# Performance work log

Hardware: AMD Instinct MI355X
Metric: run time of the kernel (lower is better)

The kernel has to match this reference:

```python
import jax, jax.numpy as jnp
import numpy as np

D_MODEL = 1024
N_HEAD = 16
D_HEAD = D_MODEL // N_HEAD
B, L = 4, 1024


def setup_inputs() -> dict:
    key = jax.random.key(0)
    ks = jax.random.split(key, 14)
    s = 0.02
    return {
        "qx": jax.random.normal(ks[0], (B, L, D_MODEL), jnp.float32),
        "kvx": jax.random.normal(ks[1], (B, L, D_MODEL), jnp.float32),
        "qs": jax.random.normal(ks[2], (B, L, D_MODEL), jnp.float32),
        "kvs": jax.random.normal(ks[3], (B, L, D_MODEL), jnp.float32),
        "w_qx1": jax.random.normal(ks[4], (D_MODEL, D_MODEL), jnp.float32) * s,
        "w_qs1": jax.random.normal(ks[5], (D_MODEL, D_MODEL), jnp.float32) * s,
        "w_qx2": jax.random.normal(ks[6], (D_MODEL, D_MODEL), jnp.float32) * s,
        "w_qs2": jax.random.normal(ks[7], (D_MODEL, D_MODEL), jnp.float32) * s,
        "w_kvx": jax.random.normal(ks[8], (D_MODEL, 2 * D_HEAD), jnp.float32) * s,
        "w_kvs": jax.random.normal(ks[9], (D_MODEL, 2 * D_HEAD), jnp.float32) * s,
        "w_xproj": jax.random.normal(ks[10], (2 * D_MODEL, D_MODEL), jnp.float32) * s,
        "b_xproj": jax.random.normal(ks[11], (D_MODEL,), jnp.float32) * s,
        "w_sproj": jax.random.normal(ks[12], (2 * D_MODEL, D_MODEL), jnp.float32) * s,
        "b_sproj": jax.random.normal(ks[13], (D_MODEL,), jnp.float32) * s,
    }


def _split_heads(t):
    # [B, L, D] -> [B, H, L, d]
    b, l, d = t.shape
    return t.reshape(b, l, N_HEAD, D_HEAD).transpose(0, 2, 1, 3)


def _merge_heads(t):
    # [B, H, L, d] -> [B, L, H*d]
    b, h, l, d = t.shape
    return t.transpose(0, 2, 1, 3).reshape(b, l, h * d)


def _attn(q, k, v):
    # q: [B, H, L, d]; k, v: [B, M, d] (single shared KV head broadcast over H)
    score = jnp.einsum("bhld,bmd->bhlm", q, k) / jnp.sqrt(jnp.float32(D_HEAD))
    p = jax.nn.softmax(score, axis=-1)
    return jnp.einsum("bhlm,bmd->bhld", p, v)


def reference(qx, kvx, qs, kvs, w_qx1, w_qs1, w_qx2, w_qs2, w_kvx, w_kvs,
              w_xproj, b_xproj, w_sproj, b_sproj):
    qx1 = _split_heads(qx @ w_qx1)
    qs1 = _split_heads(qs @ w_qs1)
    qx2 = _split_heads(qx @ w_qx2)
    qs2 = _split_heads(qs @ w_qs2)
    kx, vx = jnp.split(kvx @ w_kvx, 2, axis=-1)  # each [B, L, d]
    ks_, vs_ = jnp.split(kvs @ w_kvs, 2, axis=-1)
    x = _attn(qx1, kx, vx)
    s = _attn(qs1, ks_, vs_)
    xs = _attn(qx2, ks_, vs_)
    sx = _attn(qs2, kx, vx)
    # concat on head-dim then merge heads -> [B, L, 2*D]
    x_cat = _merge_heads(jnp.concatenate((xs, x), axis=-1))
    s_cat = _merge_heads(jnp.concatenate((sx, s), axis=-1))
    x_out = x_cat @ w_xproj + b_xproj
    s_out = s_cat @ w_sproj + b_sproj
    return (x_out, s_out)
```

## Files before the change

### kernel.cpp

```cpp
#include <hip/hip_runtime.h>
#include <hip/hip_bf16.h>


typedef short short8 __attribute__((ext_vector_type(8)));
typedef short short4v __attribute__((ext_vector_type(4)));
typedef float floatx4 __attribute__((ext_vector_type(4)));
typedef float floatx16 __attribute__((ext_vector_type(16)));
typedef unsigned uintx2 __attribute__((ext_vector_type(2)));

__device__ __forceinline__ float b2f(ushort h) {
    union { unsigned u; float f; } v; v.u = ((unsigned)h) << 16; return v.f;
}
__device__ __forceinline__ ushort f2bf(float f) {
    union { float f; unsigned u; } v; v.f = f;
    return (ushort)((v.u + 0x7FFFu + ((v.u >> 16) & 1u)) >> 16);
}
__device__ __forceinline__ unsigned cvt_pk_bf16(float lo, float hi) {
    unsigned r;
    asm("v_cvt_pk_bf16_f32 %0, %1, %2" : "=v"(r) : "v"(lo), "v"(hi));
    return r;
}
__device__ __forceinline__ void gl_lds16(const ushort* g, ushort* l) {
    __builtin_amdgcn_global_load_lds(
        (const __attribute__((address_space(1))) void*)g,
        (__attribute__((address_space(3))) void*)l, 16, 0, 0);
}

struct CB { const float* src[2]; ushort* dst[2]; };

__global__ __launch_bounds__(256) void castb(CB cb) {
    const int z = blockIdx.z;
    const float* s = cb.src[z];
    ushort* d = cb.dst[z];
    const size_t i = ((size_t)blockIdx.x * 256 + threadIdx.x) * 4;
    floatx4 f = *(const floatx4*)&s[i];
    short4v o;
#pragma unroll
    for (int k = 0; k < 4; k++) o[k] = (short)f2bf(f[k]);
    *(short4v*)&d[i] = o;
}

struct TB { const float* src[4]; ushort* dst[4]; int K[4]; int N[4]; };

__global__ __launch_bounds__(256) void tbatch(TB tb) {
    __shared__ float tile[32][33];
    const int wi = blockIdx.z;
    const int K = tb.K[wi], N = tb.N[wi];
    const int k0 = blockIdx.x * 32, n0 = blockIdx.y * 32;
    if (k0 >= K || n0 >= N) return;
    const float* W = tb.src[wi];
    ushort* Wt = tb.dst[wi];
    const int tx = threadIdx.x & 31, ty = threadIdx.x >> 5;
#pragma unroll
    for (int i = ty; i < 32; i += 8)
        tile[i][tx] = W[(size_t)(k0 + i) * N + n0 + tx];
    __syncthreads();
#pragma unroll
    for (int i = ty; i < 32; i += 8)
        Wt[(size_t)(n0 + i) * K + k0 + tx] = f2bf(tile[tx][i]);
}

__global__ __launch_bounds__(256) void gemm_q(
    const ushort* __restrict__ A, const ushort* __restrict__ Bt,
    ushort* __restrict__ C, float cscale)
{
    __shared__ ushort As[128 * 32];
    __shared__ ushort Bs[64 * 32];
    const int t = threadIdx.x;
    const int lane = t & 63, w = t >> 6;
    const int q = lane >> 4, li = lane & 15;
    const int rowA = blockIdx.x * 128, colB = blockIdx.y * 64;
    const int ar = rowA + w * 32 + (lane >> 2);
    const int br = colB + w * 16 + (lane >> 2);
    const int cl = (lane & 3) * 8;
    ushort* adst = &As[w * 32 * 32];
    ushort* bdst = &Bs[w * 16 * 32];

    floatx4 acc[2][4];
    const floatx4 z4 = {0.f, 0.f, 0.f, 0.f};
#pragma unroll
    for (int i = 0; i < 2; i++)
#pragma unroll
        for (int j = 0; j < 4; j++) acc[i][j] = z4;

    for (int k0 = 0; k0 < 1024; k0 += 32) {
        gl_lds16(A + (size_t)ar * 1024 + k0 + cl, adst);
        gl_lds16(A + (size_t)(ar + 16) * 1024 + k0 + cl, adst + 16 * 32);
        gl_lds16(Bt + (size_t)br * 1024 + k0 + cl, bdst);
        __syncthreads();
        short8 af[2], bf[4];
#pragma unroll
        for (int i = 0; i < 2; i++) af[i] = *(const short8*)&As[(w * 32 + i * 16 + li) * 32 + q * 8];
#pragma unroll
        for (int j = 0; j < 4; j++) bf[j] = *(const short8*)&Bs[(j * 16 + li) * 32 + q * 8];
#pragma unroll
        for (int i = 0; i < 2; i++)
#pragma unroll
            for (int j = 0; j < 4; j++)
                acc[i][j] = __builtin_amdgcn_mfma_f32_16x16x32_bf16(af[i], bf[j], acc[i][j], 0, 0, 0);
        __syncthreads();
    }
#pragma unroll
    for (int i = 0; i < 2; i++) {
        const int rowb = rowA + w * 32 + i * 16 + q * 4;
#pragma unroll
        for (int j = 0; j < 4; j++) {
            const int col = colB + j * 16 + li;
#pragma unroll
            for (int r = 0; r < 4; r++)
                C[(size_t)(rowb + r) * 2048 + col] = f2bf(acc[i][j][r] * cscale);
        }
    }
}

__global__ __launch_bounds__(256) void gemm_kv(
    const ushort* __restrict__ A0, const ushort* __restrict__ A1,
    const ushort* __restrict__ B0, const ushort* __restrict__ B1,
    ushort* __restrict__ C0, ushort* __restrict__ C1,
    ushort* __restrict__ vt0, ushort* __restrict__ vt1)
{
    __shared__ ushort As[128 * 32];
    __shared__ ushort Bs[128 * 32];
    const int z = blockIdx.z;
    const ushort* A = z ? A1 : A0;
    const ushort* Bt = z ? B1 : B0;
    ushort* Kp = z ? C1 : C0;
    ushort* vt = z ? vt1 : vt0;

    const int t = threadIdx.x;
    const int lane = t & 63, w = t >> 6;
    const int q = lane >> 4, li = lane & 15;
    const int wr = (w >> 1) * 64, wc = (w & 1) * 64;
    const int rowA = blockIdx.x * 128;
    const int ar = rowA + w * 32 + (lane >> 2);
    const int br = w * 32 + (lane >> 2);
    const int cl = (lane & 3) * 8;
    ushort* adst = &As[w * 32 * 32];
    ushort* bdst = &Bs[w * 32 * 32];

    floatx4 acc[4][4];
    const floatx4 z4 = {0.f, 0.f, 0.f, 0.f};
#pragma unroll
    for (int i = 0; i < 4; i++)
#pragma unroll
        for (int j = 0; j < 4; j++) acc[i][j] = z4;

    for (int k0 = 0; k0 < 1024; k0 += 32) {
        gl_lds16(A + (size_t)ar * 1024 + k0 + cl, adst);
        gl_lds16(A + (size_t)(ar + 16) * 1024 + k0 + cl, adst + 16 * 32);
        gl_lds16(Bt + (size_t)br * 1024 + k0 + cl, bdst);
        gl_lds16(Bt + (size_t)(br + 16) * 1024 + k0 + cl, bdst + 16 * 32);
        __syncthreads();
        short8 af[4], bf[4];
#pragma unroll
        for (int i = 0; i < 4; i++) af[i] = *(const short8*)&As[(wr + i * 16 + li) * 32 + q * 8];
#pragma unroll
        for (int j = 0; j < 4; j++) bf[j] = *(const short8*)&Bs[(wc + j * 16 + li) * 32 + q * 8];
#pragma unroll
        for (int i = 0; i < 4; i++)
#pragma unroll
            for (int j = 0; j < 4; j++)
                acc[i][j] = __builtin_amdgcn_mfma_f32_16x16x32_bf16(af[i], bf[j], acc[i][j], 0, 0, 0);
        __syncthreads();
    }
#pragma unroll
    for (int i = 0; i < 4; i++) {
        const int rowb = rowA + wr + i * 16 + q * 4;
#pragma unroll
        for (int j = 0; j < 4; j++) {
            const int col = wc + j * 16 + li;
#pragma unroll
            for (int r = 0; r < 4; r++) {
                const int row = rowb + r;
                const ushort vb = f2bf(acc[i][j][r]);
                if (col < 64) Kp[(size_t)row * 64 + col] = vb;
                else vt[((row >> 10) << 16) + ((col - 64) << 10) + (row & 1023)] = vb;
            }
        }
    }
}

__global__ __launch_bounds__(256) void gemm_proj(
    const ushort* __restrict__ A1, const ushort* __restrict__ A2,
    const ushort* __restrict__ Bt, const float* __restrict__ bias,
    float* __restrict__ C)
{
    __shared__ ushort As[128 * 32];
    __shared__ ushort Bs[64 * 32];
    const int t = threadIdx.x;
    const int lane = t & 63, w = t >> 6;
    const int q = lane >> 4, li = lane & 15;
    const int rowA = blockIdx.x * 128, colB = blockIdx.y * 64;
    const int ar = rowA + w * 32 + (lane >> 2);
    const int br = colB + w * 16 + (lane >> 2);
    const int cl = (lane & 3) * 8;
    ushort* adst = &As[w * 32 * 32];
    ushort* bdst = &Bs[w * 16 * 32];

    floatx4 acc[2][4];
    const floatx4 z4 = {0.f, 0.f, 0.f, 0.f};
#pragma unroll
    for (int i = 0; i < 2; i++)
#pragma unroll
        for (int j = 0; j < 4; j++) acc[i][j] = z4;

    for (int k0 = 0; k0 < 2048; k0 += 32) {
        const ushort* Ap = (k0 < 1024) ? A1 : A2;
        const int kc = k0 & 1023;
        const int kp = kc + cl;
        const int ks = ((kp >> 6) << 7) + (kp & 63) + ((k0 >= 1024) ? 64 : 0);
        gl_lds16(Ap + (size_t)ar * 1024 + kc + cl, adst);
        gl_lds16(Ap + (size_t)(ar + 16) * 1024 + kc + cl, adst + 16 * 32);
        gl_lds16(Bt + (size_t)br * 2048 + ks, bdst);
        __syncthreads();
        short8 af[2], bf[4];
#pragma unroll
        for (int i = 0; i < 2; i++) af[i] = *(const short8*)&As[(w * 32 + i * 16 + li) * 32 + q * 8];
#pragma unroll
        for (int j = 0; j < 4; j++) bf[j] = *(const short8*)&Bs[(j * 16 + li) * 32 + q * 8];
#pragma unroll
        for (int i = 0; i < 2; i++)
#pragma unroll
            for (int j = 0; j < 4; j++)
                acc[i][j] = __builtin_amdgcn_mfma_f32_16x16x32_bf16(af[i], bf[j], acc[i][j], 0, 0, 0);
        __syncthreads();
    }
#pragma unroll
    for (int i = 0; i < 2; i++) {
        const int rowb = rowA + w * 32 + i * 16 + q * 4;
#pragma unroll
        for (int j = 0; j < 4; j++) {
            const int col = colB + j * 16 + li;
            const float bv = bias[col];
#pragma unroll
            for (int r = 0; r < 4; r++)
                C[(size_t)(rowb + r) * 1024 + col] = acc[i][j][r] + bv;
        }
    }
}

__global__ __launch_bounds__(256, 4) void attn_kernel(
    const ushort* __restrict__ Qbase,
    const ushort* __restrict__ KVa, const ushort* __restrict__ KVb,
    ushort* __restrict__ OutA, ushort* __restrict__ OutB)
{
    __shared__ ushort Kt[64 * 68];
    __shared__ ushort Vt[64 * 68];
    __shared__ __align__(16) float Ls[4][32];

    const int t = threadIdx.x;
    const int lane = t & 63, w = t >> 6;
    const int ql = lane & 31, hi = lane >> 5;
    const int qt = blockIdx.x, h = blockIdx.y;
    const int z = blockIdx.z, b = z >> 1, a2 = z & 1;

    const ushort* Q  = Qbase + (a2 ? 1024 : 0);
    const ushort* KV = a2 ? KVb : KVa;
    ushort* Out      = a2 ? OutB : OutA;
    const ushort* Kp = KV;
    const ushort* Vg = KV + 262144;

    const size_t qrow = (size_t)(b * 1024 + qt * 128 + w * 32 + ql);
    short8 qf[4];
#pragma unroll
    for (int dc = 0; dc < 4; dc++)
        qf[dc] = *(const short8*)&Q[qrow * 2048 + h * 64 + dc * 16 + hi * 8];

    float lsum = 0.f;
    floatx16 accO[2];
#pragma unroll
    for (int dt = 0; dt < 2; dt++)
#pragma unroll
        for (int i = 0; i < 16; i++) accO[dt][i] = 0.f;

    const int srow = t >> 2, sch = (t & 3) * 16;
    const ushort* ksrc0 = &Kp[(size_t)(b * 1024 + srow) * 64 + sch];
    const ushort* vsrc0 = &Vg[(size_t)(b * 64 + srow) * 1024 + sch];
    ushort* kdst = &Kt[srow * 68 + sch];
    ushort* vdst = &Vt[srow * 68 + sch];

    short8 kreg[2], vreg[2];
#pragma unroll
    for (int i = 0; i < 2; i++) {
        kreg[i] = *(const short8*)&ksrc0[i * 8];
        vreg[i] = *(const short8*)&vsrc0[i * 8];
    }

    for (int kt = 0; kt < 16; kt++) {
#pragma unroll
        for (int i = 0; i < 2; i++) {
            *(short8*)&kdst[i * 8] = kreg[i];
            *(short8*)&vdst[i * 8] = vreg[i];
        }
        __syncthreads();

        if (kt < 15) {
            const ushort* ksrc = ksrc0 + (size_t)(kt + 1) * 64 * 64;
            const ushort* vsrc = vsrc0 + (kt + 1) * 64;
#pragma unroll
            for (int i = 0; i < 2; i++) {
                kreg[i] = *(const short8*)&ksrc[i * 8];
                vreg[i] = *(const short8*)&vsrc[i * 8];
            }
        }

#pragma unroll
        for (int ktile = 0; ktile < 2; ktile++) {
            floatx16 S;
#pragma unroll
            for (int i = 0; i < 16; i++) S[i] = 0.f;
            __builtin_amdgcn_s_setprio(1);
#pragma unroll
            for (int dc = 0; dc < 4; dc++) {
                short8 kf = *(const short8*)&Kt[(ktile * 32 + ql) * 68 + dc * 16 + hi * 8];
                S = __builtin_amdgcn_mfma_f32_32x32x16_bf16(kf, qf[dc], S, 0, 0, 0);
            }
            __builtin_amdgcn_s_setprio(0);

            float e[16];
#pragma unroll
            for (int r = 0; r < 16; r++) e[r] = exp2f(S[r]);
            float sa = (e[0] + e[1]) + (e[2] + e[3]);
            float sb = (e[4] + e[5]) + (e[6] + e[7]);
            float sc = (e[8] + e[9]) + (e[10] + e[11]);
            float sd = (e[12] + e[13]) + (e[14] + e[15]);
            lsum += (sa + sb) + (sc + sd);

#pragma unroll
            for (int p = 0; p < 2; p++) {
                unsigned cA = cvt_pk_bf16(e[8 * p + 0], e[8 * p + 1]);
                unsigned cC = cvt_pk_bf16(e[8 * p + 2], e[8 * p + 3]);
                unsigned cB = cvt_pk_bf16(e[8 * p + 4], e[8 * p + 5]);
                unsigned cD = cvt_pk_bf16(e[8 * p + 6], e[8 * p + 7]);
                uintx2 s02 = __builtin_amdgcn_permlane32_swap(cA, cB, false, false);
                uintx2 s13 = __builtin_amdgcn_permlane32_swap(cC, cD, false, false);
                union { unsigned u[4]; short8 s; } pf;
                pf.u[0] = s02[0]; pf.u[1] = s13[0];
                pf.u[2] = s02[1]; pf.u[3] = s13[1];
                const int kslot = ktile * 2 + p;
                __builtin_amdgcn_s_setprio(1);
#pragma unroll
                for (int dt = 0; dt < 2; dt++) {
                    short8 vf = *(const short8*)&Vt[(dt * 32 + ql) * 68 + kslot * 16 + hi * 8];
                    accO[dt] = __builtin_amdgcn_mfma_f32_32x32x16_bf16(pf.s, vf, accO[dt], 0, 0, 0);
                }
                __builtin_amdgcn_s_setprio(0);
            }
        }
        __syncthreads();
    }

    lsum += __shfl_xor(lsum, 32);
    Ls[w][ql] = lsum;

    const int orow0 = b * 1024 + qt * 128 + w * 32;
#pragma unroll
    for (int g = 0; g < 4; g++) {
        floatx4 L4 = *(const floatx4*)&Ls[w][g * 8 + hi * 4];
#pragma unroll
        for (int rr = 0; rr < 4; rr++) {
            const float inv = 1.f / L4[rr];
            const int row = orow0 + g * 8 + hi * 4 + rr;
#pragma unroll
            for (int dt = 0; dt < 2; dt++)
                Out[(size_t)row * 1024 + h * 64 + dt * 32 + ql] =
                    f2bf(accO[dt][g * 4 + rr] * inv);
        }
    }
}

extern "C" void kernel_launch(void* const* d_in, const int* in_sizes, int n_in,
                              void* d_out, int out_size, void* d_ws, size_t ws_size,
                              hipStream_t stream) {
    const float* qx    = (const float*)d_in[0];
    const float* kvx   = (const float*)d_in[1];
    const float* qs    = (const float*)d_in[2];
    const float* kvs   = (const float*)d_in[3];
    const float* w_qx1 = (const float*)d_in[4];
    const float* w_qs1 = (const float*)d_in[5];
    const float* w_qx2 = (const float*)d_in[6];
    const float* w_qs2 = (const float*)d_in[7];
    const float* w_kvx = (const float*)d_in[8];
    const float* w_kvs = (const float*)d_in[9];
    const float* w_xp  = (const float*)d_in[10];
    const float* b_xp  = (const float*)d_in[11];
    const float* w_sp  = (const float*)d_in[12];
    const float* b_sp  = (const float*)d_in[13];
    float* out = (float*)d_out;
    (void)ws_size; (void)in_sizes; (void)n_in; (void)out_size;

    ushort* ws   = (ushort*)d_ws;
    ushort* Wb   = ws;
    ushort* q1q2 = ws + 4194304;
    ushort* Mbuf = ws + 12582912;
    ushort* kvpx = ws + 16777216;
    ushort* kvps = ws + 17301504;

    const float qsc = 0.125f * 1.44269504088896f;

    CB c1; c1.src[0] = kvx; c1.dst[0] = Mbuf; c1.src[1] = kvs; c1.dst[1] = q1q2;
    castb<<<dim3(4096, 1, 2), 256, 0, stream>>>(c1);

    TB tb1;
    tb1.src[0] = w_kvx; tb1.dst[0] = Wb;           tb1.K[0] = 1024; tb1.N[0] = 128;
    tb1.src[1] = w_kvs; tb1.dst[1] = Wb + 131072;  tb1.K[1] = 1024; tb1.N[1] = 128;
    tb1.src[2] = w_qs1; tb1.dst[2] = Wb + 262144;  tb1.K[2] = 1024; tb1.N[2] = 1024;
    tb1.src[3] = w_qs2; tb1.dst[3] = Wb + 1310720; tb1.K[3] = 1024; tb1.N[3] = 1024;
    tbatch<<<dim3(32, 32, 4), 256, 0, stream>>>(tb1);

    gemm_kv<<<dim3(32, 1, 2), 256, 0, stream>>>(
        Mbuf, q1q2, Wb, Wb + 131072, kvpx, kvps, kvpx + 262144, kvps + 262144);

    CB c2; c2.src[0] = qs; c2.dst[0] = Mbuf; c2.src[1] = qs; c2.dst[1] = Mbuf;
    castb<<<dim3(4096, 1, 1), 256, 0, stream>>>(c2);

    gemm_q<<<dim3(32, 32), 256, 0, stream>>>(Mbuf, Wb + 262144, q1q2, qsc);

    attn_kernel<<<dim3(8, 16, 8), 256, 0, stream>>>(q1q2, kvps, kvpx, Mbuf, (ushort*)out);

    TB tb2;
    tb2.src[0] = w_sp;  tb2.dst[0] = Wb;           tb2.K[0] = 2048; tb2.N[0] = 1024;
    tb2.src[1] = w_qx1; tb2.dst[1] = Wb + 2097152; tb2.K[1] = 1024; tb2.N[1] = 1024;
    tb2.src[2] = w_qx2; tb2.dst[2] = Wb + 3145728; tb2.K[2] = 1024; tb2.N[2] = 1024;
    tb2.src[3] = w_sp;  tb2.dst[3] = Wb;           tb2.K[3] = 0;    tb2.N[3] = 0;
    tbatch<<<dim3(64, 32, 3), 256, 0, stream>>>(tb2);

    gemm_proj<<<dim3(32, 16), 256, 0, stream>>>((ushort*)out, Mbuf, Wb, b_sp, out + 4194304);

    CB c3; c3.src[0] = qx; c3.dst[0] = Mbuf; c3.src[1] = qx; c3.dst[1] = Mbuf;
    castb<<<dim3(4096, 1, 1), 256, 0, stream>>>(c3);

    gemm_q<<<dim3(32, 32), 256, 0, stream>>>(Mbuf, Wb + 2097152, q1q2, qsc);

    attn_kernel<<<dim3(8, 16, 8), 256, 0, stream>>>(q1q2, kvpx, kvps, Mbuf, Wb);

    TB tb3;
    tb3.src[0] = w_xp; tb3.dst[0] = q1q2; tb3.K[0] = 2048; tb3.N[0] = 1024;
    tb3.src[1] = w_xp; tb3.dst[1] = q1q2; tb3.K[1] = 0;    tb3.N[1] = 0;
    tb3.src[2] = w_xp; tb3.dst[2] = q1q2; tb3.K[2] = 0;    tb3.N[2] = 0;
    tb3.src[3] = w_xp; tb3.dst[3] = q1q2; tb3.K[3] = 0;    tb3.N[3] = 0;
    tbatch<<<dim3(64, 32, 1), 256, 0, stream>>>(tb3);

    gemm_proj<<<dim3(32, 16), 256, 0, stream>>>(Wb, Mbuf, q1q2, b_xp, out);
}
```

Measured before the change: 449.1 us.

## Double K-step per barrier in GEMMs and switch attention exp to __expf

The q-projection and output-projection GEMMs now load two 32-wide K slices per iteration into separate LDS buffers and run both MFMA groups between one pair of barriers. This halves the number of synchronisations and loop iterations and keeps more loads in flight, at the cost of twice the LDS per block. Separately, the attention softmax uses __expf on unscaled-by-log2e scores instead of exp2f on pre-scaled scores. __expf likely lowers to exp2 plus a multiply, which adds a multiply per element for no clear gain.

```diff
diff --git a/kernel.cpp b/kernel.cpp
--- a/kernel.cpp
+++ b/kernel.cpp
@@ -64,8 +64,10 @@
     const ushort* __restrict__ A, const ushort* __restrict__ Bt,
     ushort* __restrict__ C, float cscale)
 {
-    __shared__ ushort As[128 * 32];
-    __shared__ ushort Bs[64 * 32];
+    __shared__ ushort As0[128 * 32];
+    __shared__ ushort As1[128 * 32];
+    __shared__ ushort Bs0[64 * 32];
+    __shared__ ushort Bs1[64 * 32];
     const int t = threadIdx.x;
     const int lane = t & 63, w = t >> 6;
     const int q = lane >> 4, li = lane & 15;
@@ -73,8 +75,10 @@
     const int ar = rowA + w * 32 + (lane >> 2);
     const int br = colB + w * 16 + (lane >> 2);
     const int cl = (lane & 3) * 8;
-    ushort* adst = &As[w * 32 * 32];
-    ushort* bdst = &Bs[w * 16 * 32];
+    ushort* adst0 = &As0[w * 32 * 32];
+    ushort* adst1 = &As1[w * 32 * 32];
+    ushort* bdst0 = &Bs0[w * 16 * 32];
+    ushort* bdst1 = &Bs1[w * 16 * 32];
 
     floatx4 acc[2][4];
     const floatx4 z4 = {0.f, 0.f, 0.f, 0.f};
@@ -83,16 +87,28 @@
 #pragma unroll
         for (int j = 0; j < 4; j++) acc[i][j] = z4;
 
-    for (int k0 = 0; k0 < 1024; k0 += 32) {
-        gl_lds16(A + (size_t)ar * 1024 + k0 + cl, adst);
-        gl_lds16(A + (size_t)(ar + 16) * 1024 + k0 + cl, adst + 16 * 32);
-        gl_lds16(Bt + (size_t)br * 1024 + k0 + cl, bdst);
+    for (int k0 = 0; k0 < 1024; k0 += 64) {
+        gl_lds16(A + (size_t)ar * 1024 + k0 + cl, adst0);
+        gl_lds16(A + (size_t)(ar + 16) * 1024 + k0 + cl, adst0 + 16 * 32);
+        gl_lds16(A + (size_t)ar * 1024 + k0 + 32 + cl, adst1);
+        gl_lds16(A + (size_t)(ar + 16) * 1024 + k0 + 32 + cl, adst1 + 16 * 32);
+        gl_lds16(Bt + (size_t)br * 1024 + k0 + cl, bdst0);
+        gl_lds16(Bt + (size_t)br * 1024 + k0 + 32 + cl, bdst1);
         __syncthreads();
         short8 af[2], bf[4];
 #pragma unroll
-        for (int i = 0; i < 2; i++) af[i] = *(const short8*)&As[(w * 32 + i * 16 + li) * 32 + q * 8];
-#pragma unroll
-        for (int j = 0; j < 4; j++) bf[j] = *(const short8*)&Bs[(j * 16 + li) * 32 + q * 8];
+        for (int i = 0; i < 2; i++) af[i] = *(const short8*)&As0[(w * 32 + i * 16 + li) * 32 + q * 8];
+#pragma unroll
+        for (int j = 0; j < 4; j++) bf[j] = *(const short8*)&Bs0[(j * 16 + li) * 32 + q * 8];
+#pragma unroll
+        for (int i = 0; i < 2; i++)
+#pragma unroll
+            for (int j = 0; j < 4; j++)
+                acc[i][j] = __builtin_amdgcn_mfma_f32_16x16x32_bf16(af[i], bf[j], acc[i][j], 0, 0, 0);
+#pragma unroll
+        for (int i = 0; i < 2; i++) af[i] = *(const short8*)&As1[(w * 32 + i * 16 + li) * 32 + q * 8];
+#pragma unroll
+        for (int j = 0; j < 4; j++) bf[j] = *(const short8*)&Bs1[(j * 16 + li) * 32 + q * 8];
 #pragma unroll
         for (int i = 0; i < 2; i++)
 #pragma unroll
@@ -185,8 +201,10 @@
     const ushort* __restrict__ Bt, const float* __restrict__ bias,
     float* __restrict__ C)
 {
-    __shared__ ushort As[128 * 32];
-    __shared__ ushort Bs[64 * 32];
+    __shared__ ushort As0[128 * 32];
+    __shared__ ushort As1[128 * 32];
+    __shared__ ushort Bs0[64 * 32];
+    __shared__ ushort Bs1[64 * 32];
     const int t = threadIdx.x;
     const int lane = t & 63, w = t >> 6;
     const int q = lane >> 4, li = lane & 15;
@@ -194,8 +212,10 @@
     const int ar = rowA + w * 32 + (lane >> 2);
     const int br = colB + w * 16 + (lane >> 2);
     const int cl = (lane & 3) * 8;
-    ushort* adst = &As[w * 32 * 32];
-    ushort* bdst = &Bs[w * 16 * 32];
+    ushort* adst0 = &As0[w * 32 * 32];
+    ushort* adst1 = &As1[w * 32 * 32];
+    ushort* bdst0 = &Bs0[w * 16 * 32];
+    ushort* bdst1 = &Bs1[w * 16 * 32];
 
     floatx4 acc[2][4];
     const floatx4 z4 = {0.f, 0.f, 0.f, 0.f};
@@ -204,20 +224,35 @@
 #pragma unroll
         for (int j = 0; j < 4; j++) acc[i][j] = z4;
 
-    for (int k0 = 0; k0 < 2048; k0 += 32) {
+    for (int k0 = 0; k0 < 2048; k0 += 64) {
         const ushort* Ap = (k0 < 1024) ? A1 : A2;
         const int kc = k0 & 1023;
-        const int kp = kc + cl;
-        const int ks = ((kp >> 6) << 7) + (kp & 63) + ((k0 >= 1024) ? 64 : 0);
-        gl_lds16(Ap + (size_t)ar * 1024 + kc + cl, adst);
-        gl_lds16(Ap + (size_t)(ar + 16) * 1024 + kc + cl, adst + 16 * 32);
-        gl_lds16(Bt + (size_t)br * 2048 + ks, bdst);
+        const int kp0 = kc + cl;
+        const int kp1 = kc + 32 + cl;
+        const int koff = (k0 >= 1024) ? 64 : 0;
+        const int ks0 = ((kp0 >> 6) << 7) + (kp0 & 63) + koff;
+        const int ks1 = ((kp1 >> 6) << 7) + (kp1 & 63) + koff;
+        gl_lds16(Ap + (size_t)ar * 1024 + kc + cl, adst0);
+        gl_lds16(Ap + (size_t)(ar + 16) * 1024 + kc + cl, adst0 + 16 * 32);
+        gl_lds16(Ap + (size_t)ar * 1024 + kc + 32 + cl, adst1);
+        gl_lds16(Ap + (size_t)(ar + 16) * 1024 + kc + 32 + cl, adst1 + 16 * 32);
+        gl_lds16(Bt + (size_t)br * 2048 + ks0, bdst0);
+        gl_lds16(Bt + (size_t)br * 2048 + ks1, bdst1);
         __syncthreads();
         short8 af[2], bf[4];
 #pragma unroll
-        for (int i = 0; i < 2; i++) af[i] = *(const short8*)&As[(w * 32 + i * 16 + li) * 32 + q * 8];
-#pragma unroll
-        for (int j = 0; j < 4; j++) bf[j] = *(const short8*)&Bs[(j * 16 + li) * 32 + q * 8];
+        for (int i = 0; i < 2; i++) af[i] = *(const short8*)&As0[(w * 32 + i * 16 + li) * 32 + q * 8];
+#pragma unroll
+        for (int j = 0; j < 4; j++) bf[j] = *(const short8*)&Bs0[(j * 16 + li) * 32 + q * 8];
+#pragma unroll
+        for (int i = 0; i < 2; i++)
+#pragma unroll
+            for (int j = 0; j < 4; j++)
+                acc[i][j] = __builtin_amdgcn_mfma_f32_16x16x32_bf16(af[i], bf[j], acc[i][j], 0, 0, 0);
+#pragma unroll
+        for (int i = 0; i < 2; i++) af[i] = *(const short8*)&As1[(w * 32 + i * 16 + li) * 32 + q * 8];
+#pragma unroll
+        for (int j = 0; j < 4; j++) bf[j] = *(const short8*)&Bs1[(j * 16 + li) * 32 + q * 8];
 #pragma unroll
         for (int i = 0; i < 2; i++)
 #pragma unroll
@@ -319,7 +354,7 @@
 
             float e[16];
 #pragma unroll
-            for (int r = 0; r < 16; r++) e[r] = exp2f(S[r]);
+            for (int r = 0; r < 16; r++) e[r] = __expf(S[r]);
             float sa = (e[0] + e[1]) + (e[2] + e[3]);
             float sb = (e[4] + e[5]) + (e[6] + e[7]);
             float sc = (e[8] + e[9]) + (e[10] + e[11]);
@@ -396,8 +431,6 @@
     ushort* kvpx = ws + 16777216;
     ushort* kvps = ws + 17301504;
 
-    const float qsc = 0.125f * 1.44269504088896f;
-
     CB c1; c1.src[0] = kvx; c1.dst[0] = Mbuf; c1.src[1] = kvs; c1.dst[1] = q1q2;
     castb<<<dim3(4096, 1, 2), 256, 0, stream>>>(c1);
 
@@ -414,7 +447,7 @@
     CB c2; c2.src[0] = qs; c2.dst[0] = Mbuf; c2.src[1] = qs; c2.dst[1] = Mbuf;
     castb<<<dim3(4096, 1, 1), 256, 0, stream>>>(c2);
 
-    gemm_q<<<dim3(32, 32), 256, 0, stream>>>(Mbuf, Wb + 262144, q1q2, qsc);
+    gemm_q<<<dim3(32, 32), 256, 0, stream>>>(Mbuf, Wb + 262144, q1q2, 0.125f);
 
     attn_kernel<<<dim3(8, 16, 8), 256, 0, stream>>>(q1q2, kvps, kvpx, Mbuf, (ushort*)out);
 
@@ -430,7 +463,7 @@
     CB c3; c3.src[0] = qx; c3.dst[0] = Mbuf; c3.src[1] = qx; c3.dst[1] = Mbuf;
     castb<<<dim3(4096, 1, 1), 256, 0, stream>>>(c3);
 
-    gemm_q<<<dim3(32, 32), 256, 0, stream>>>(Mbuf, Wb + 2097152, q1q2, qsc);
+    gemm_q<<<dim3(32, 32), 256, 0, stream>>>(Mbuf, Wb + 2097152, q1q2, 0.125f);
 
     attn_kernel<<<dim3(8, 16, 8), 256, 0, stream>>>(q1q2, kvpx, kvps, Mbuf, Wb);
 
```

Result: faster. 417.5 us (-7.0%).

## Double-buffer LDS in Q and projection GEMMs with 64-wide K steps

Applied to the files above, without the earlier changes.

The Q-projection and output-projection GEMMs now use two LDS buffers and stage 64 K-elements per iteration. The next tile's global-to-LDS loads are issued while the current tile is being multiplied, and there is one barrier per iteration instead of two. This targets the serialized load-then-compute pattern. It also removes the log2(e) factor from the Q scale and switches the attention exponent from exp2f to __expf, which may compile to an extra multiply before the exp2. LDS use per block grows fourfold, which could reduce occupancy.

```diff
diff --git a/kernel.cpp b/kernel.cpp
--- a/kernel.cpp
+++ b/kernel.cpp
@@ -64,8 +64,8 @@
     const ushort* __restrict__ A, const ushort* __restrict__ Bt,
     ushort* __restrict__ C, float cscale)
 {
-    __shared__ ushort As[128 * 32];
-    __shared__ ushort Bs[64 * 32];
+    __shared__ ushort As[2][2][128 * 32];
+    __shared__ ushort Bs[2][2][64 * 32];
     const int t = threadIdx.x;
     const int lane = t & 63, w = t >> 6;
     const int q = lane >> 4, li = lane & 15;
@@ -73,8 +73,6 @@
     const int ar = rowA + w * 32 + (lane >> 2);
     const int br = colB + w * 16 + (lane >> 2);
     const int cl = (lane & 3) * 8;
-    ushort* adst = &As[w * 32 * 32];
-    ushort* bdst = &Bs[w * 16 * 32];
 
     floatx4 acc[2][4];
     const floatx4 z4 = {0.f, 0.f, 0.f, 0.f};
@@ -83,22 +81,35 @@
 #pragma unroll
         for (int j = 0; j < 4; j++) acc[i][j] = z4;
 
-    for (int k0 = 0; k0 < 1024; k0 += 32) {
-        gl_lds16(A + (size_t)ar * 1024 + k0 + cl, adst);
-        gl_lds16(A + (size_t)(ar + 16) * 1024 + k0 + cl, adst + 16 * 32);
-        gl_lds16(Bt + (size_t)br * 1024 + k0 + cl, bdst);
-        __syncthreads();
+    auto stage = [&](int ph, int k0) {
+        gl_lds16(A + (size_t)ar * 1024 + k0 + cl,        &As[ph][0][w * 32 * 32]);
+        gl_lds16(A + (size_t)(ar + 16) * 1024 + k0 + cl, &As[ph][0][w * 32 * 32] + 16 * 32);
+        gl_lds16(A + (size_t)ar * 1024 + k0 + 32 + cl,        &As[ph][1][w * 32 * 32]);
+        gl_lds16(A + (size_t)(ar + 16) * 1024 + k0 + 32 + cl, &As[ph][1][w * 32 * 32] + 16 * 32);
+        gl_lds16(Bt + (size_t)br * 1024 + k0 + cl,      &Bs[ph][0][w * 16 * 32]);
+        gl_lds16(Bt + (size_t)br * 1024 + k0 + 32 + cl, &Bs[ph][1][w * 16 * 32]);
+    };
+
+    stage(0, 0);
+    for (int it = 0; it < 16; it++) {
+        const int cur = it & 1;
+        __syncthreads();
+        if (it < 15) stage(cur ^ 1, (it + 1) * 64);
         short8 af[2], bf[4];
 #pragma unroll
-        for (int i = 0; i < 2; i++) af[i] = *(const short8*)&As[(w * 32 + i * 16 + li) * 32 + q * 8];
-#pragma unroll
-        for (int j = 0; j < 4; j++) bf[j] = *(const short8*)&Bs[(j * 16 + li) * 32 + q * 8];
-#pragma unroll
-        for (int i = 0; i < 2; i++)
+        for (int ks = 0; ks < 2; ks++) {
+#pragma unroll
+            for (int i = 0; i < 2; i++)
+                af[i] = *(const short8*)&As[cur][ks][(w * 32 + i * 16 + li) * 32 + q * 8];
 #pragma unroll
             for (int j = 0; j < 4; j++)
-                acc[i][j] = __builtin_amdgcn_mfma_f32_16x16x32_bf16(af[i], bf[j], acc[i][j], 0, 0, 0);
-        __syncthreads();
+                bf[j] = *(const short8*)&Bs[cur][ks][(j * 16 + li) * 32 + q * 8];
+#pragma unroll
+            for (int i = 0; i < 2; i++)
+#pragma unroll
+                for (int j = 0; j < 4; j++)
+                    acc[i][j] = __builtin_amdgcn_mfma_f32_16x16x32_bf16(af[i], bf[j], acc[i][j], 0, 0, 0);
+        }
     }
 #pragma unroll
     for (int i = 0; i < 2; i++) {
@@ -185,8 +196,8 @@
     const ushort* __restrict__ Bt, const float* __restrict__ bias,
     float* __restrict__ C)
 {
-    __shared__ ushort As[128 * 32];
-    __shared__ ushort Bs[64 * 32];
+    __shared__ ushort As[2][2][128 * 32];
+    __shared__ ushort Bs[2][2][64 * 32];
     const int t = threadIdx.x;
     const int lane = t & 63, w = t >> 6;
     const int q = lane >> 4, li = lane & 15;
@@ -194,8 +205,6 @@
     const int ar = rowA + w * 32 + (lane >> 2);
     const int br = colB + w * 16 + (lane >> 2);
     const int cl = (lane & 3) * 8;
-    ushort* adst = &As[w * 32 * 32];
-    ushort* bdst = &Bs[w * 16 * 32];
 
     floatx4 acc[2][4];
     const floatx4 z4 = {0.f, 0.f, 0.f, 0.f};
@@ -204,26 +213,42 @@
 #pragma unroll
         for (int j = 0; j < 4; j++) acc[i][j] = z4;
 
-    for (int k0 = 0; k0 < 2048; k0 += 32) {
+    auto stage = [&](int ph, int k0) {
         const ushort* Ap = (k0 < 1024) ? A1 : A2;
         const int kc = k0 & 1023;
-        const int kp = kc + cl;
-        const int ks = ((kp >> 6) << 7) + (kp & 63) + ((k0 >= 1024) ? 64 : 0);
-        gl_lds16(Ap + (size_t)ar * 1024 + kc + cl, adst);
-        gl_lds16(Ap + (size_t)(ar + 16) * 1024 + kc + cl, adst + 16 * 32);
-        gl_lds16(Bt + (size_t)br * 2048 + ks, bdst);
-        __syncthreads();
+        const int koff = (k0 >= 1024) ? 64 : 0;
+        const int kp0 = kc + cl;
+        const int kp1 = kc + 32 + cl;
+        const int ks0 = ((kp0 >> 6) << 7) + (kp0 & 63) + koff;
+        const int ks1 = ((kp1 >> 6) << 7) + (kp1 & 63) + koff;
+        gl_lds16(Ap + (size_t)ar * 1024 + kc + cl,        &As[ph][0][w * 32 * 32]);
+        gl_lds16(Ap + (size_t)(ar + 16) * 1024 + kc + cl, &As[ph][0][w * 32 * 32] + 16 * 32);
+        gl_lds16(Ap + (size_t)ar * 1024 + kc + 32 + cl,        &As[ph][1][w * 32 * 32]);
+        gl_lds16(Ap + (size_t)(ar + 16) * 1024 + kc + 32 + cl, &As[ph][1][w * 32 * 32] + 16 * 32);
+        gl_lds16(Bt + (size_t)br * 2048 + ks0, &Bs[ph][0][w * 16 * 32]);
+        gl_lds16(Bt + (size_t)br * 2048 + ks1, &Bs[ph][1][w * 16 * 32]);
+    };
+
+    stage(0, 0);
+    for (int it = 0; it < 32; it++) {
+        const int cur = it & 1;
+        __syncthreads();
+        if (it < 31) stage(cur ^ 1, (it + 1) * 64);
         short8 af[2], bf[4];
 #pragma unroll
-        for (int i = 0; i < 2; i++) af[i] = *(const short8*)&As[(w * 32 + i * 16 + li) * 32 + q * 8];
-#pragma unroll
-        for (int j = 0; j < 4; j++) bf[j] = *(const short8*)&Bs[(j * 16 + li) * 32 + q * 8];
-#pragma unroll
-        for (int i = 0; i < 2; i++)
+        for (int ks = 0; ks < 2; ks++) {
+#pragma unroll
+            for (int i = 0; i < 2; i++)
+                af[i] = *(const short8*)&As[cur][ks][(w * 32 + i * 16 + li) * 32 + q * 8];
 #pragma unroll
             for (int j = 0; j < 4; j++)
-                acc[i][j] = __builtin_amdgcn_mfma_f32_16x16x32_bf16(af[i], bf[j], acc[i][j], 0, 0, 0);
-        __syncthreads();
+                bf[j] = *(const short8*)&Bs[cur][ks][(j * 16 + li) * 32 + q * 8];
+#pragma unroll
+            for (int i = 0; i < 2; i++)
+#pragma unroll
+                for (int j = 0; j < 4; j++)
+                    acc[i][j] = __builtin_amdgcn_mfma_f32_16x16x32_bf16(af[i], bf[j], acc[i][j], 0, 0, 0);
+        }
     }
 #pragma unroll
     for (int i = 0; i < 2; i++) {
@@ -319,7 +344,7 @@
 
             float e[16];
 #pragma unroll
-            for (int r = 0; r < 16; r++) e[r] = exp2f(S[r]);
+            for (int r = 0; r < 16; r++) e[r] = __expf(S[r]);
             float sa = (e[0] + e[1]) + (e[2] + e[3]);
             float sb = (e[4] + e[5]) + (e[6] + e[7]);
             float sc = (e[8] + e[9]) + (e[10] + e[11]);
@@ -396,8 +421,6 @@
     ushort* kvpx = ws + 16777216;
     ushort* kvps = ws + 17301504;
 
-    const float qsc = 0.125f * 1.44269504088896f;
-
     CB c1; c1.src[0] = kvx; c1.dst[0] = Mbuf; c1.src[1] = kvs; c1.dst[1] = q1q2;
     castb<<<dim3(4096, 1, 2), 256, 0, stream>>>(c1);
 
@@ -414,7 +437,7 @@
     CB c2; c2.src[0] = qs; c2.dst[0] = Mbuf; c2.src[1] = qs; c2.dst[1] = Mbuf;
     castb<<<dim3(4096, 1, 1), 256, 0, stream>>>(c2);
 
-    gemm_q<<<dim3(32, 32), 256, 0, stream>>>(Mbuf, Wb + 262144, q1q2, qsc);
+    gemm_q<<<dim3(32, 32), 256, 0, stream>>>(Mbuf, Wb + 262144, q1q2, 0.125f);
 
     attn_kernel<<<dim3(8, 16, 8), 256, 0, stream>>>(q1q2, kvps, kvpx, Mbuf, (ushort*)out);
 
@@ -430,7 +453,7 @@
     CB c3; c3.src[0] = qx; c3.dst[0] = Mbuf; c3.src[1] = qx; c3.dst[1] = Mbuf;
     castb<<<dim3(4096, 1, 1), 256, 0, stream>>>(c3);
 
-    gemm_q<<<dim3(32, 32), 256, 0, stream>>>(Mbuf, Wb + 2097152, q1q2, qsc);
+    gemm_q<<<dim3(32, 32), 256, 0, stream>>>(Mbuf, Wb + 2097152, q1q2, 0.125f);
 
     attn_kernel<<<dim3(8, 16, 8), 256, 0, stream>>>(q1q2, kvpx, kvps, Mbuf, Wb);
 
```

Measured after the change: 436.5 us. 1.03x faster.
